# Kernel optimization log

Measured on AMD Instinct MI355X. Metric: run time of the kernel, lower is better.

The kernel has to match this reference:

```python
import jax, jax.numpy as jnp
import numpy as np

LAMBDA_M = 1.0
NUM_GRU_LAYERS = 3

B, S, H, G = 64, 512, 768, 768


def setup_inputs() -> dict:
    key = jax.random.key(0)
    ks = jax.random.split(key, 12)
    std = 0.02
    # variable-length attention mask (all rows non-empty)
    lengths = jax.random.randint(ks[0], (B,), S // 4, S + 1)
    attention_mask = (jnp.arange(S)[None, :] < lengths[:, None]).astype(jnp.float32)
    return {
        "sentence_representation": jax.random.normal(ks[1], (B, H), jnp.float32),
        "attention_mask": attention_mask,
        "aspect_embedding": jax.random.normal(ks[2], (B, H), jnp.float32),
        "sentence_embeddings": jax.random.normal(ks[3], (B, S, H), jnp.float32),
        "ws": std * jax.random.normal(ks[4], (H, H), jnp.float32),
        "wa": std * jax.random.normal(ks[5], (H, H), jnp.float32),
        "w": std * jax.random.normal(ks[6], (H,), jnp.float32),
        "whs": std * jax.random.normal(ks[7], (H, G), jnp.float32),
        "wd1": std * jax.random.normal(ks[8], (H, H), jnp.float32),
        "wd": std * jax.random.normal(ks[9], (G, H), jnp.float32),
        "w_ih": std * jax.random.normal(ks[10], (3 * G, H), jnp.float32),  # GRU input weights (r,z,n)
        "w_hh": std * jax.random.normal(ks[11], (3 * G, G), jnp.float32),  # GRU hidden weights (r,z,n)
    }


def _gru_cell(x, h, w_ih, w_hh):
    # standard GRU cell, bias=False (torch gate order: r, z, n)
    gi = x @ w_ih.T  # (B, 3G)
    gh = h @ w_hh.T  # (B, 3G)
    i_r, i_z, i_n = jnp.split(gi, 3, axis=-1)
    h_r, h_z, h_n = jnp.split(gh, 3, axis=-1)
    r = jax.nn.sigmoid(i_r + h_r)
    z = jax.nn.sigmoid(i_z + h_z)
    n = jnp.tanh(i_n + r * h_n)
    return (1.0 - z) * n + z * h


def reference(sentence_representation, attention_mask, aspect_embedding,
              sentence_embeddings, ws, wa, w, whs, wd1, wd, w_ih, w_hh):
    # Hoist loop-invariant projections (same math as recomputing per layer)
    Se = jnp.einsum('bsh,hk->bsk', sentence_embeddings, ws)  # (B,S,H)
    A = aspect_embedding @ wa                                 # (B,H)
    mask = attention_mask                                     # (B,S)
    denom = mask.sum(-1, keepdims=True)                       # (B,1)
    h = sentence_representation
    for t in range(NUM_GRU_LAYERS):
        Wd = wd1 if t == 0 else wd
        M = Se + (h @ Wd)[:, None, :] + A[:, None, :]         # (B,S,H)
        scores = jnp.tanh(M) @ w                              # (B,S)
        m = jax.nn.softmax(LAMBDA_M * scores, axis=-1)        # (B,S)
        # reweighted masked-mean pooling
        at = jnp.einsum('bs,bsh->bh', m * mask, sentence_embeddings) / denom
        if t == 0:
            h = h @ whs                                       # project to GRU hidden dim
        h = _gru_cell(at, h, w_ih, w_hh)
    return h
```

## Files before the change

kernel.cpp:

```cpp
#include <hip/hip_runtime.h>
#include <hip/hip_bf16.h>
#include <stdint.h>

#define Bdim 64
#define Sdim 512
#define Hdim 768
#define G3   2304

typedef float f32x4 __attribute__((ext_vector_type(4)));
typedef short s16x8 __attribute__((ext_vector_type(8)));
typedef short s16x4 __attribute__((ext_vector_type(4)));

__device__ __forceinline__ float bf2f(unsigned short u){
  union { unsigned int i; float f; } c; c.i = ((unsigned int)u) << 16; return c.f;
}
__device__ __forceinline__ unsigned short f2bf(float f){
  union { float f; unsigned int i; } c; c.f = f;
  unsigned int x = c.i;
  return (unsigned short)((x + 0x7fffu + ((x >> 16) & 1u)) >> 16);
}
__device__ __forceinline__ float fast_tanh(float x){
  float e = __expf(2.f * x);
  return 1.f - 2.f / (e + 1.f);
}
__device__ __forceinline__ float fast_sigmoid(float x){
  return 1.f / (1.f + __expf(-x));
}
__device__ __forceinline__ void gload16(const void* g, void* l){
  __builtin_amdgcn_global_load_lds((const __attribute__((address_space(1))) void*)g,
                                   (__attribute__((address_space(3))) void*)l, 16, 0, 0);
}

__global__ __launch_bounds__(256) void k_prep(const float* __restrict__ SE, unsigned short* __restrict__ SEb,
                                              const float* __restrict__ ws_, unsigned short* __restrict__ wsbT,
                                              const float* __restrict__ wd1, unsigned short* __restrict__ wd1T,
                                              const float* __restrict__ wd,  unsigned short* __restrict__ wdT,
                                              const float* __restrict__ wa,  unsigned short* __restrict__ waT,
                                              const float* __restrict__ whs, unsigned short* __restrict__ whsT,
                                              const float* __restrict__ w_ih, unsigned short* __restrict__ w_ihb,
                                              const float* __restrict__ w_hh, unsigned short* __restrict__ w_hhb,
                                              const float* __restrict__ sr,  unsigned short* __restrict__ srb,
                                              const float* __restrict__ asp, unsigned short* __restrict__ aspb){
  __shared__ float tile[32][33];
  int bid = blockIdx.x;
  if (bid < 2880) {
    int which = bid / 576, r = bid % 576;
    const float* src; unsigned short* dst;
    switch (which) {
      case 0: src = ws_; dst = wsbT; break;
      case 1: src = wd1; dst = wd1T; break;
      case 2: src = wd;  dst = wdT;  break;
      case 3: src = wa;  dst = waT;  break;
      default: src = whs; dst = whsT; break;
    }
    int bx = (r % 24) * 32, by = (r / 24) * 32;
    int tx = threadIdx.x % 32, ty = threadIdx.x / 32;
    for (int j = ty; j < 32; j += 8) tile[j][tx] = src[(size_t)(by + j) * Hdim + bx + tx];
    __syncthreads();
    for (int j = ty; j < 32; j += 8) dst[(size_t)(bx + j) * Hdim + by + tx] = f2bf(tile[tx][j]);
    return;
  }
  bid -= 2880;
  const float* s; unsigned short* d; int j;
  if      (bid < 12288) { s = SE;   d = SEb;   j = bid * 256 + threadIdx.x; }
  else if (bid < 13152) { s = w_ih; d = w_ihb; j = (bid - 12288) * 256 + threadIdx.x; }
  else if (bid < 14016) { s = w_hh; d = w_hhb; j = (bid - 13152) * 256 + threadIdx.x; }
  else if (bid < 14040) { s = sr;   d = srb;   j = (bid - 14016) * 256 + threadIdx.x; }
  else                  { s = asp;  d = aspb;  j = (bid - 14040) * 256 + threadIdx.x; }
  const float4* sp = (const float4*)s;
  float4 a = sp[2*j], b = sp[2*j+1];
  uint4 o;
  o.x = (unsigned)f2bf(a.x) | ((unsigned)f2bf(a.y) << 16);
  o.y = (unsigned)f2bf(a.z) | ((unsigned)f2bf(a.w) << 16);
  o.z = (unsigned)f2bf(b.x) | ((unsigned)f2bf(b.y) << 16);
  o.w = (unsigned)f2bf(b.z) | ((unsigned)f2bf(b.w) << 16);
  ((uint4*)d)[j] = o;
}

__global__ __launch_bounds__(256) void k_conv_bf16(const float* __restrict__ src,
                                                   unsigned short* __restrict__ dst, int n8){
  int i = blockIdx.x * 256 + threadIdx.x;
  if (i >= n8) return;
  const float4* s = (const float4*)src;
  float4 a = s[2*i], b = s[2*i+1];
  uint4 o;
  o.x = (unsigned)f2bf(a.x) | ((unsigned)f2bf(a.y) << 16);
  o.y = (unsigned)f2bf(a.z) | ((unsigned)f2bf(a.w) << 16);
  o.z = (unsigned)f2bf(b.x) | ((unsigned)f2bf(b.y) << 16);
  o.w = (unsigned)f2bf(b.z) | ((unsigned)f2bf(b.w) << 16);
  ((uint4*)dst)[i] = o;
}

__global__ __launch_bounds__(256) void k_conv4(const float* __restrict__ s0, unsigned short* __restrict__ d0, int c0,
                                               const float* __restrict__ s1, unsigned short* __restrict__ d1, int c1,
                                               const float* __restrict__ s2, unsigned short* __restrict__ d2, int c2,
                                               const float* __restrict__ s3, unsigned short* __restrict__ d3, int c3){
  int i = blockIdx.x * 256 + threadIdx.x;
  const float* s; unsigned short* d; int j;
  if (i < c0) { s = s0; d = d0; j = i; }
  else if (i < c0 + c1) { s = s1; d = d1; j = i - c0; }
  else if (i < c0 + c1 + c2) { s = s2; d = d2; j = i - c0 - c1; }
  else if (i < c0 + c1 + c2 + c3) { s = s3; d = d3; j = i - c0 - c1 - c2; }
  else return;
  const float4* sp = (const float4*)s;
  float4 a = sp[2*j], b = sp[2*j+1];
  uint4 o;
  o.x = (unsigned)f2bf(a.x) | ((unsigned)f2bf(a.y) << 16);
  o.y = (unsigned)f2bf(a.z) | ((unsigned)f2bf(a.w) << 16);
  o.z = (unsigned)f2bf(b.x) | ((unsigned)f2bf(b.y) << 16);
  o.w = (unsigned)f2bf(b.z) | ((unsigned)f2bf(b.w) << 16);
  ((uint4*)d)[j] = o;
}

__global__ __launch_bounds__(256) void k_transpose_ws(const float* __restrict__ src,
                                                      unsigned short* __restrict__ dst){
  __shared__ float tile[32][33];
  int bx = blockIdx.x * 32, by = blockIdx.y * 32;
  int tx = threadIdx.x % 32, ty = threadIdx.x / 32;
  for (int j = ty; j < 32; j += 8) tile[j][tx] = src[(size_t)(by + j) * Hdim + bx + tx];
  __syncthreads();
  for (int j = ty; j < 32; j += 8) dst[(size_t)(bx + j) * Hdim + by + tx] = f2bf(tile[tx][j]);
}

__global__ __launch_bounds__(256) void k_transpose4(const float* __restrict__ s0, unsigned short* __restrict__ d0,
                                                    const float* __restrict__ s1, unsigned short* __restrict__ d1,
                                                    const float* __restrict__ s2, unsigned short* __restrict__ d2,
                                                    const float* __restrict__ s3, unsigned short* __restrict__ d3){
  const float* src; unsigned short* dst;
  switch (blockIdx.z) {
    case 0: src = s0; dst = d0; break;
    case 1: src = s1; dst = d1; break;
    case 2: src = s2; dst = d2; break;
    default: src = s3; dst = d3; break;
  }
  __shared__ float tile[32][33];
  int bx = blockIdx.x * 32, by = blockIdx.y * 32;
  int tx = threadIdx.x % 32, ty = threadIdx.x / 32;
  for (int j = ty; j < 32; j += 8) tile[j][tx] = src[(size_t)(by + j) * Hdim + bx + tx];
  __syncthreads();
  for (int j = ty; j < 32; j += 8) dst[(size_t)(bx + j) * Hdim + by + tx] = f2bf(tile[tx][j]);
}

__global__ __launch_bounds__(256) void k_gemm_se(const unsigned short* __restrict__ A,
                                                 const unsigned short* __restrict__ Bt,
                                                 unsigned short* __restrict__ C){
  __shared__ unsigned short As[128 * 64];
  __shared__ unsigned short Bs[128 * 64];
  const int t = threadIdx.x;
  const int lane = t & 63;
  const int w = t >> 6, wr = w >> 1, wc = w & 1;
  int bid = blockIdx.x;
  int swz = (bid & 7) * 192 + (bid >> 3);
  const int m0 = (swz / 6) * 128, n0 = (swz % 6) * 128;

  f32x4 acc[4][4];
  #pragma unroll
  for (int m = 0; m < 4; m++)
    #pragma unroll
    for (int n = 0; n < 4; n++) acc[m][n] = (f32x4){0.f, 0.f, 0.f, 0.f};

  for (int k0 = 0; k0 < Hdim; k0 += 64) {
    #pragma unroll
    for (int i = 0; i < 4; i++) {
      int L = t * 16 + i * 4096;
      int row = L >> 7;
      int offp = L & 127;
      int goff = offp ^ ((row & 7) << 4);
      int wub = __builtin_amdgcn_readfirstlane((t & 192) * 16 + i * 4096);
      gload16((const char*)A  + ((size_t)(m0 + row) * Hdim + k0) * 2 + goff, (char*)As + wub);
      gload16((const char*)Bt + ((size_t)(n0 + row) * Hdim + k0) * 2 + goff, (char*)Bs + wub);
    }
    __syncthreads();
    #pragma unroll
    for (int kk = 0; kk < 2; kk++) {
      s16x8 af[4], bfr[4];
      #pragma unroll
      for (int m = 0; m < 4; m++) {
        int row = wr * 64 + m * 16 + (lane & 15);
        int sw = (row & 7) << 4;
        int kb = kk * 64 + (lane >> 4) * 8;
        s16x4 lo = *(const s16x4*)((const char*)As + row * 128 + (kb ^ sw));
        s16x4 hi = *(const s16x4*)((const char*)As + row * 128 + ((kb + 32) ^ sw));
        af[m] = __builtin_shufflevector(lo, hi, 0, 1, 2, 3, 4, 5, 6, 7);
      }
      #pragma unroll
      for (int n = 0; n < 4; n++) {
        int row = wc * 64 + n * 16 + (lane & 15);
        int sw = (row & 7) << 4;
        int kb = kk * 64 + (lane >> 4) * 8;
        s16x4 lo = *(const s16x4*)((const char*)Bs + row * 128 + (kb ^ sw));
        s16x4 hi = *(const s16x4*)((const char*)Bs + row * 128 + ((kb + 32) ^ sw));
        bfr[n] = __builtin_shufflevector(lo, hi, 0, 1, 2, 3, 4, 5, 6, 7);
      }
      #pragma unroll
      for (int m = 0; m < 4; m++)
        #pragma unroll
        for (int n = 0; n < 4; n++)
          acc[m][n] = __builtin_amdgcn_mfma_f32_16x16x32_bf16(af[m], bfr[n], acc[m][n], 0, 0, 0);
    }
    __syncthreads();
  }
  #pragma unroll
  for (int m = 0; m < 4; m++) {
    int rowb = m0 + wr * 64 + m * 16 + (lane >> 4) * 4;
    #pragma unroll
    for (int n = 0; n < 4; n++) {
      int col = n0 + wc * 64 + n * 16 + (lane & 15);
      #pragma unroll
      for (int r = 0; r < 4; r++)
        C[(size_t)(rowb + r) * Hdim + col] = f2bf(acc[m][n][r]);
    }
  }
}

__device__ __forceinline__ void smallM_body(const unsigned short* __restrict__ A,
                                            const unsigned short* __restrict__ Bt,
                                            float* __restrict__ C, unsigned short* __restrict__ Cb,
                                            char* ldsbuf, int n0){
  unsigned short* As = (unsigned short*)ldsbuf;
  unsigned short* Bs = (unsigned short*)(ldsbuf + 8192);
  const int t = threadIdx.x, lane = t & 63, w = t >> 6;
  f32x4 acc[4][2];
  #pragma unroll
  for (int m = 0; m < 4; m++)
    #pragma unroll
    for (int n = 0; n < 2; n++) acc[m][n] = (f32x4){0.f, 0.f, 0.f, 0.f};

  for (int k0 = 0; k0 < Hdim; k0 += 64) {
    #pragma unroll
    for (int i = 0; i < 2; i++) {
      int L = t * 16 + i * 4096, row = L >> 7, off = L & 127;
      *(uint4*)((char*)As + row * 128 + (off ^ ((row & 7) << 4))) =
        *(const uint4*)((const char*)A + ((size_t)row * Hdim + k0) * 2 + off);
    }
    #pragma unroll
    for (int i = 0; i < 4; i++) {
      int L = t * 16 + i * 4096, row = L >> 7, off = L & 127;
      *(uint4*)((char*)Bs + row * 128 + (off ^ ((row & 7) << 4))) =
        *(const uint4*)((const char*)Bt + ((size_t)(n0 + row) * Hdim + k0) * 2 + off);
    }
    __syncthreads();
    #pragma unroll
    for (int kk = 0; kk < 2; kk++) {
      s16x8 af[4], bfr[2];
      int kb = kk * 64 + (lane >> 4) * 8;
      #pragma unroll
      for (int m = 0; m < 4; m++) {
        int row = m * 16 + (lane & 15);
        int sw = (row & 7) << 4;
        s16x4 lo = *(const s16x4*)((const char*)As + row * 128 + (kb ^ sw));
        s16x4 hi = *(const s16x4*)((const char*)As + row * 128 + ((kb + 32) ^ sw));
        af[m] = __builtin_shufflevector(lo, hi, 0, 1, 2, 3, 4, 5, 6, 7);
      }
      #pragma unroll
      for (int n = 0; n < 2; n++) {
        int row = w * 32 + n * 16 + (lane & 15);
        int sw = (row & 7) << 4;
        s16x4 lo = *(const s16x4*)((const char*)Bs + row * 128 + (kb ^ sw));
        s16x4 hi = *(const s16x4*)((const char*)Bs + row * 128 + ((kb + 32) ^ sw));
        bfr[n] = __builtin_shufflevector(lo, hi, 0, 1, 2, 3, 4, 5, 6, 7);
      }
      #pragma unroll
      for (int m = 0; m < 4; m++)
        #pragma unroll
        for (int n = 0; n < 2; n++)
          acc[m][n] = __builtin_amdgcn_mfma_f32_16x16x32_bf16(af[m], bfr[n], acc[m][n], 0, 0, 0);
    }
    __syncthreads();
  }
  #pragma unroll
  for (int m = 0; m < 4; m++) {
    int rowb = m * 16 + (lane >> 4) * 4;
    #pragma unroll
    for (int n = 0; n < 2; n++) {
      int col = n0 + w * 32 + n * 16 + (lane & 15);
      #pragma unroll
      for (int r = 0; r < 4; r++) {
        float v = acc[m][n][r];
        C[(size_t)(rowb + r) * Hdim + col] = v;
        if (Cb) Cb[(size_t)(rowb + r) * Hdim + col] = f2bf(v);
      }
    }
  }
}

__device__ __forceinline__ void vpart_body(const unsigned short* __restrict__ A1,
                                           const unsigned short* __restrict__ B1t,
                                           const unsigned short* __restrict__ A2,
                                           const unsigned short* __restrict__ B2t,
                                           float* __restrict__ Vp,
                                           char* ldsbuf, int n0, int kc){
  unsigned short* As = (unsigned short*)ldsbuf;
  unsigned short* Bs = (unsigned short*)(ldsbuf + 8192);
  const int t = threadIdx.x, lane = t & 63, w = t >> 6;
  f32x4 acc[4][2];
  #pragma unroll
  for (int m = 0; m < 4; m++)
    #pragma unroll
    for (int n = 0; n < 2; n++) acc[m][n] = (f32x4){0.f, 0.f, 0.f, 0.f};

  #pragma unroll
  for (int gi = 0; gi < 4; gi++) {
    int g = kc * 4 + gi;
    const unsigned short* A  = (g < 12) ? A1 : A2;
    const unsigned short* Bt = (g < 12) ? B1t : B2t;
    int k0 = (g % 12) * 64;
    #pragma unroll
    for (int i = 0; i < 2; i++) {
      int L = t * 16 + i * 4096, row = L >> 7, off = L & 127;
      *(uint4*)((char*)As + row * 128 + (off ^ ((row & 7) << 4))) =
        *(const uint4*)((const char*)A + ((size_t)row * Hdim + k0) * 2 + off);
    }
    #pragma unroll
    for (int i = 0; i < 4; i++) {
      int L = t * 16 + i * 4096, row = L >> 7, off = L & 127;
      *(uint4*)((char*)Bs + row * 128 + (off ^ ((row & 7) << 4))) =
        *(const uint4*)((const char*)Bt + ((size_t)(n0 + row) * Hdim + k0) * 2 + off);
    }
    __syncthreads();
    #pragma unroll
    for (int kk = 0; kk < 2; kk++) {
      s16x8 af[4], bfr[2];
      int kb = kk * 64 + (lane >> 4) * 8;
      #pragma unroll
      for (int m = 0; m < 4; m++) {
        int row = m * 16 + (lane & 15);
        int sw = (row & 7) << 4;
        s16x4 lo = *(const s16x4*)((const char*)As + row * 128 + (kb ^ sw));
        s16x4 hi = *(const s16x4*)((const char*)As + row * 128 + ((kb + 32) ^ sw));
        af[m] = __builtin_shufflevector(lo, hi, 0, 1, 2, 3, 4, 5, 6, 7);
      }
      #pragma unroll
      for (int n = 0; n < 2; n++) {
        int row = w * 32 + n * 16 + (lane & 15);
        int sw = (row & 7) << 4;
        s16x4 lo = *(const s16x4*)((const char*)Bs + row * 128 + (kb ^ sw));
        s16x4 hi = *(const s16x4*)((const char*)Bs + row * 128 + ((kb + 32) ^ sw));
        bfr[n] = __builtin_shufflevector(lo, hi, 0, 1, 2, 3, 4, 5, 6, 7);
      }
      #pragma unroll
      for (int m = 0; m < 4; m++)
        #pragma unroll
        for (int n = 0; n < 2; n++)
          acc[m][n] = __builtin_amdgcn_mfma_f32_16x16x32_bf16(af[m], bfr[n], acc[m][n], 0, 0, 0);
    }
    __syncthreads();
  }
  float* outp = Vp + (size_t)kc * (Bdim * Hdim);
  #pragma unroll
  for (int m = 0; m < 4; m++) {
    int rowb = m * 16 + (lane >> 4) * 4;
    #pragma unroll
    for (int n = 0; n < 2; n++) {
      int col = n0 + w * 32 + n * 16 + (lane & 15);
      #pragma unroll
      for (int r = 0; r < 4; r++)
        outp[(size_t)(rowb + r) * Hdim + col] = acc[m][n][r];
    }
  }
}

__global__ __launch_bounds__(256) void k_vpart(const unsigned short* __restrict__ A1,
                                               const unsigned short* __restrict__ B1t,
                                               const unsigned short* __restrict__ A2,
                                               const unsigned short* __restrict__ B2t,
                                               float* __restrict__ Vp){
  __shared__ char lds[24576];
  vpart_body(A1, B1t, A2, B2t, Vp, lds, blockIdx.x * 128, blockIdx.y);
}

__global__ __launch_bounds__(256) void k_init2(const unsigned short* __restrict__ srb,
                                               const unsigned short* __restrict__ whsT,
                                               float* __restrict__ hA, unsigned short* __restrict__ hbA,
                                               const unsigned short* __restrict__ wd1T,
                                               const unsigned short* __restrict__ aspb,
                                               const unsigned short* __restrict__ waT,
                                               float* __restrict__ Vp){
  __shared__ char lds[24576];
  if (blockIdx.y == 6) smallM_body(srb, whsT, hA, hbA, lds, blockIdx.x * 128);
  else                 vpart_body(srb, wd1T, aspb, waT, Vp, lds, blockIdx.x * 128, blockIdx.y);
}

__global__ __launch_bounds__(256) void k_scores(const unsigned short* __restrict__ Seb,
                                                const float* __restrict__ Vp,
                                                const float* __restrict__ wv,
                                                float* __restrict__ scores){
  int b = blockIdx.y;
  int s_base = blockIdx.x * 16;
  int t = threadIdx.x, lane = t & 63, w = t >> 6;
  f32x4 v0 = {0,0,0,0}, v1 = {0,0,0,0}, v2 = {0,0,0,0};
  #pragma unroll
  for (int kc = 0; kc < 6; kc++) {
    const float* Vb = Vp + ((size_t)kc * Bdim + b) * Hdim;
    v0 += *(const f32x4*)(Vb + lane * 8);
    v1 += *(const f32x4*)(Vb + lane * 8 + 4);
    v2 += *(const f32x4*)(Vb + 512 + lane * 4);
  }
  f32x4 w0 = *(const f32x4*)(wv + lane * 8);
  f32x4 w1 = *(const f32x4*)(wv + lane * 8 + 4);
  f32x4 w2 = *(const f32x4*)(wv + 512 + lane * 4);
  #pragma unroll
  for (int si = 0; si < 4; si++) {
    int s = s_base + w * 4 + si;
    const unsigned short* rp = Seb + ((size_t)b * Sdim + s) * Hdim;
    ushort4 p0 = *(const ushort4*)(rp + lane * 8);
    ushort4 p1 = *(const ushort4*)(rp + lane * 8 + 4);
    ushort4 p2 = *(const ushort4*)(rp + 512 + lane * 4);
    float acc;
    acc  = fast_tanh(bf2f(p0.x) + v0[0]) * w0[0];
    acc += fast_tanh(bf2f(p0.y) + v0[1]) * w0[1];
    acc += fast_tanh(bf2f(p0.z) + v0[2]) * w0[2];
    acc += fast_tanh(bf2f(p0.w) + v0[3]) * w0[3];
    acc += fast_tanh(bf2f(p1.x) + v1[0]) * w1[0];
    acc += fast_tanh(bf2f(p1.y) + v1[1]) * w1[1];
    acc += fast_tanh(bf2f(p1.z) + v1[2]) * w1[2];
    acc += fast_tanh(bf2f(p1.w) + v1[3]) * w1[3];
    acc += fast_tanh(bf2f(p2.x) + v2[0]) * w2[0];
    acc += fast_tanh(bf2f(p2.y) + v2[1]) * w2[1];
    acc += fast_tanh(bf2f(p2.z) + v2[2]) * w2[2];
    acc += fast_tanh(bf2f(p2.w) + v2[3]) * w2[3];
    #pragma unroll
    for (int o = 32; o; o >>= 1) acc += __shfl_xor(acc, o);
    if (lane == 0) scores[(size_t)b * Sdim + s] = acc;
  }
}

__global__ __launch_bounds__(192) void k_at_sm_bf16(const unsigned short* __restrict__ SEb,
                                                    const float* __restrict__ scores,
                                                    const float* __restrict__ mask,
                                                    float* __restrict__ at_part){
  int sc = blockIdx.x, b = blockIdx.y;
  int t = threadIdx.x, lane = t & 63, w = t >> 6;
  __shared__ float sbuf[512];
  __shared__ float mbuf[512];
  __shared__ float red[3], red2[3];
  __shared__ float msh[64];
  __shared__ float half0[96 * 8];
  float lmax = -1e30f;
  #pragma unroll
  for (int j = 0; j < 3; j++) {
    int idx = t + 192 * j;
    if (idx < 512) {
      float v = scores[(size_t)b * Sdim + idx];
      float mk = mask[(size_t)b * Sdim + idx];
      sbuf[idx] = v; mbuf[idx] = mk;
      lmax = fmaxf(lmax, v);
    }
  }
  #pragma unroll
  for (int o = 32; o; o >>= 1) lmax = fmaxf(lmax, __shfl_xor(lmax, o));
  if (lane == 0) red[w] = lmax;
  __syncthreads();
  float mx = fmaxf(fmaxf(red[0], red[1]), red[2]);
  float le = 0.f, lm = 0.f;
  #pragma unroll
  for (int j = 0; j < 3; j++) {
    int idx = t + 192 * j;
    if (idx < 512) {
      float e = __expf(sbuf[idx] - mx);
      le += e; lm += mbuf[idx];
      sbuf[idx] = e * mbuf[idx];
    }
  }
  #pragma unroll
  for (int o = 32; o; o >>= 1) { le += __shfl_xor(le, o); lm += __shfl_xor(lm, o); }
  __syncthreads();
  if (lane == 0) { red[w] = le; red2[w] = lm; }
  __syncthreads();
  float inv = 1.f / ((red[0] + red[1] + red[2]) * (red2[0] + red2[1] + red2[2]));
  if (t < 64) msh[t] = sbuf[sc * 64 + t] * inv;
  __syncthreads();
  int hseg = t % 96, sh = t / 96;
  const unsigned short* base = SEb + ((size_t)b * Sdim + sc * 64 + sh * 32) * Hdim + hseg * 8;
  float acc[8] = {0, 0, 0, 0, 0, 0, 0, 0};
  for (int s = 0; s < 32; s++) {
    float m = msh[sh * 32 + s];
    ushort4 a = *(const ushort4*)(base + (size_t)s * Hdim);
    ushort4 c = *(const ushort4*)(base + (size_t)s * Hdim + 4);
    acc[0] += m * bf2f(a.x); acc[1] += m * bf2f(a.y); acc[2] += m * bf2f(a.z); acc[3] += m * bf2f(a.w);
    acc[4] += m * bf2f(c.x); acc[5] += m * bf2f(c.y); acc[6] += m * bf2f(c.z); acc[7] += m * bf2f(c.w);
  }
  if (sh == 0) {
    #pragma unroll
    for (int j = 0; j < 8; j++) half0[hseg * 8 + j] = acc[j];
  }
  __syncthreads();
  if (sh == 1) {
    float* op = at_part + ((size_t)sc * Bdim + b) * Hdim + hseg * 8;
    #pragma unroll
    for (int j = 0; j < 8; j++) op[j] = acc[j] + half0[hseg * 8 + j];
  }
}

__global__ __launch_bounds__(192) void k_at_sm_f32(const float* __restrict__ SE,
                                                   const float* __restrict__ scores,
                                                   const float* __restrict__ mask,
                                                   float* __restrict__ at_part){
  int sc = blockIdx.x, b = blockIdx.y;
  int t = threadIdx.x, lane = t & 63, w = t >> 6;
  __shared__ float sbuf[512];
  __shared__ float mbuf[512];
  __shared__ float red[3], red2[3];
  __shared__ float msh[64];
  __shared__ float half0[96 * 8];
  float lmax = -1e30f;
  #pragma unroll
  for (int j = 0; j < 3; j++) {
    int idx = t + 192 * j;
    if (idx < 512) {
      float v = scores[(size_t)b * Sdim + idx];
      float mk = mask[(size_t)b * Sdim + idx];
      sbuf[idx] = v; mbuf[idx] = mk;
      lmax = fmaxf(lmax, v);
    }
  }
  #pragma unroll
  for (int o = 32; o; o >>= 1) lmax = fmaxf(lmax, __shfl_xor(lmax, o));
  if (lane == 0) red[w] = lmax;
  __syncthreads();
  float mx = fmaxf(fmaxf(red[0], red[1]), red[2]);
  float le = 0.f, lm = 0.f;
  #pragma unroll
  for (int j = 0; j < 3; j++) {
    int idx = t + 192 * j;
    if (idx < 512) {
      float e = __expf(sbuf[idx] - mx);
      le += e; lm += mbuf[idx];
      sbuf[idx] = e * mbuf[idx];
    }
  }
  #pragma unroll
  for (int o = 32; o; o >>= 1) { le += __shfl_xor(le, o); lm += __shfl_xor(lm, o); }
  __syncthreads();
  if (lane == 0) { red[w] = le; red2[w] = lm; }
  __syncthreads();
  float inv = 1.f / ((red[0] + red[1] + red[2]) * (red2[0] + red2[1] + red2[2]));
  if (t < 64) msh[t] = sbuf[sc * 64 + t] * inv;
  __syncthreads();
  int hseg = t % 96, sh = t / 96;
  const float* base = SE + ((size_t)b * Sdim + sc * 64 + sh * 32) * Hdim + hseg * 8;
  float acc[8] = {0, 0, 0, 0, 0, 0, 0, 0};
  for (int s = 0; s < 32; s++) {
    float m = msh[sh * 32 + s];
    float4 a = *(const float4*)(base + (size_t)s * Hdim);
    float4 c = *(const float4*)(base + (size_t)s * Hdim + 4);
    acc[0] += m * a.x; acc[1] += m * a.y; acc[2] += m * a.z; acc[3] += m * a.w;
    acc[4] += m * c.x; acc[5] += m * c.y; acc[6] += m * c.z; acc[7] += m * c.w;
  }
  if (sh == 0) {
    #pragma unroll
    for (int j = 0; j < 8; j++) half0[hseg * 8 + j] = acc[j];
  }
  __syncthreads();
  if (sh == 1) {
    float* op = at_part + ((size_t)sc * Bdim + b) * Hdim + hseg * 8;
    #pragma unroll
    for (int j = 0; j < 8; j++) op[j] = acc[j] + half0[hseg * 8 + j];
  }
}

__global__ __launch_bounds__(256) void k_at_reduce(const float* __restrict__ at_part,
                                                   unsigned short* __restrict__ atb){
  int i = blockIdx.x * 256 + threadIdx.x;
  float s = 0.f;
  #pragma unroll
  for (int p = 0; p < 8; p++) s += at_part[(size_t)p * (Bdim * Hdim) + i];
  atb[i] = f2bf(s);
}

__global__ __launch_bounds__(256) void k_gates2(const unsigned short* __restrict__ atb,
                                                const unsigned short* __restrict__ hb,
                                                const unsigned short* __restrict__ w_ihb,
                                                const unsigned short* __restrict__ w_hhb,
                                                float* __restrict__ gi2,
                                                float* __restrict__ gh2){
  __shared__ unsigned short As[64 * 64];
  __shared__ unsigned short Bs[128 * 64];
  const int t = threadIdx.x, lane = t & 63, w = t >> 6;
  const int n0 = blockIdx.x * 128;
  const int z = blockIdx.y, kc = blockIdx.z;
  const unsigned short* A  = z ? hb : atb;
  const unsigned short* Bt = z ? w_hhb : w_ihb;
  float* outp = (z ? gh2 : gi2) + (size_t)kc * (Bdim * G3);
  f32x4 acc[4][2];
  #pragma unroll
  for (int m = 0; m < 4; m++)
    #pragma unroll
    for (int n = 0; n < 2; n++) acc[m][n] = (f32x4){0.f, 0.f, 0.f, 0.f};

  for (int it = 0; it < 6; it++) {
    int k0 = kc * 384 + it * 64;
    #pragma unroll
    for (int i = 0; i < 2; i++) {
      int L = t * 16 + i * 4096, row = L >> 7, off = L & 127;
      *(uint4*)((char*)As + row * 128 + (off ^ ((row & 7) << 4))) =
        *(const uint4*)((const char*)A + ((size_t)row * Hdim + k0) * 2 + off);
    }
    #pragma unroll
    for (int i = 0; i < 4; i++) {
      int L = t * 16 + i * 4096, row = L >> 7, off = L & 127;
      *(uint4*)((char*)Bs + row * 128 + (off ^ ((row & 7) << 4))) =
        *(const uint4*)((const char*)Bt + ((size_t)(n0 + row) * Hdim + k0) * 2 + off);
    }
    __syncthreads();
    #pragma unroll
    for (int kk = 0; kk < 2; kk++) {
      s16x8 af[4], bfr[2];
      int kb = kk * 64 + (lane >> 4) * 8;
      #pragma unroll
      for (int m = 0; m < 4; m++) {
        int row = m * 16 + (lane & 15);
        int sw = (row & 7) << 4;
        s16x4 lo = *(const s16x4*)((const char*)As + row * 128 + (kb ^ sw));
        s16x4 hi = *(const s16x4*)((const char*)As + row * 128 + ((kb + 32) ^ sw));
        af[m] = __builtin_shufflevector(lo, hi, 0, 1, 2, 3, 4, 5, 6, 7);
      }
      #pragma unroll
      for (int n = 0; n < 2; n++) {
        int row = w * 32 + n * 16 + (lane & 15);
        int sw = (row & 7) << 4;
        s16x4 lo = *(const s16x4*)((const char*)Bs + row * 128 + (kb ^ sw));
        s16x4 hi = *(const s16x4*)((const char*)Bs + row * 128 + ((kb + 32) ^ sw));
        bfr[n] = __builtin_shufflevector(lo, hi, 0, 1, 2, 3, 4, 5, 6, 7);
      }
      #pragma unroll
      for (int m = 0; m < 4; m++)
        #pragma unroll
        for (int n = 0; n < 2; n++)
          acc[m][n] = __builtin_amdgcn_mfma_f32_16x16x32_bf16(af[m], bfr[n], acc[m][n], 0, 0, 0);
    }
    __syncthreads();
  }
  #pragma unroll
  for (int m = 0; m < 4; m++) {
    int rowb = m * 16 + (lane >> 4) * 4;
    #pragma unroll
    for (int n = 0; n < 2; n++) {
      int col = n0 + w * 32 + n * 16 + (lane & 15);
      #pragma unroll
      for (int r = 0; r < 4; r++)
        outp[(size_t)(rowb + r) * G3 + col] = acc[m][n][r];
    }
  }
}

__global__ __launch_bounds__(256) void k_gru_elem2(const float* __restrict__ gi2,
                                                   const float* __restrict__ gh2,
                                                   const float* __restrict__ h,
                                                   float* __restrict__ hout,
                                                   unsigned short* __restrict__ hbout){
  int i = blockIdx.x * 256 + threadIdx.x;
  int b = i / Hdim, g = i % Hdim;
  const size_t P = (size_t)Bdim * G3;
  const float* gia = gi2 + (size_t)b * G3;
  const float* gha = gh2 + (size_t)b * G3;
  float ir = gia[g] + gia[P + g];
  float iz = gia[Hdim + g] + gia[P + Hdim + g];
  float in_ = gia[2 * Hdim + g] + gia[P + 2 * Hdim + g];
  float hr = gha[g] + gha[P + g];
  float hz = gha[Hdim + g] + gha[P + Hdim + g];
  float hn = gha[2 * Hdim + g] + gha[P + 2 * Hdim + g];
  float r = fast_sigmoid(ir + hr);
  float z = fast_sigmoid(iz + hz);
  float n = fast_tanh(in_ + r * hn);
  float ho = (1.f - z) * n + z * h[i];
  hout[i] = ho;
  hbout[i] = f2bf(ho);
}

extern "C" void kernel_launch(void* const* d_in, const int* in_sizes, int n_in,
                              void* d_out, int out_size, void* d_ws, size_t ws_size,
                              hipStream_t stream) {
  const float* sr   = (const float*)d_in[0];
  const float* mask = (const float*)d_in[1];
  const float* asp  = (const float*)d_in[2];
  const float* SE   = (const float*)d_in[3];
  const float* ws_  = (const float*)d_in[4];
  const float* wa   = (const float*)d_in[5];
  const float* wv   = (const float*)d_in[6];
  const float* whs  = (const float*)d_in[7];
  const float* wd1  = (const float*)d_in[8];
  const float* wd   = (const float*)d_in[9];
  const float* w_ih = (const float*)d_in[10];
  const float* w_hh = (const float*)d_in[11];
  float* out = (float*)d_out;

  char* p = (char*)d_ws;
  size_t offA = 0;
  auto A_ = [&](size_t b) -> char* { char* r = p + offA; offA += b; return r; };
  unsigned short* Seb  = (unsigned short*)A_(50331648);
  unsigned short* wsbT = (unsigned short*)A_(1179648);
  unsigned short* SEb  = (unsigned short*)A_(50331648);

  const size_t othersBytes = 18100224;
  bool keepSEb = (offA + othersBytes) <= ws_size;
  char* q = keepSEb ? (p + offA) : (char*)SEb;
  size_t o2 = 0;
  auto B_ = [&](size_t b) -> char* { char* r = q + o2; o2 += b; return r; };
  unsigned short* w_ihb = (unsigned short*)B_(3538944);
  unsigned short* w_hhb = (unsigned short*)B_(3538944);
  unsigned short* wd1T  = (unsigned short*)B_(1179648);
  unsigned short* wdT   = (unsigned short*)B_(1179648);
  unsigned short* waT   = (unsigned short*)B_(1179648);
  unsigned short* whsT  = (unsigned short*)B_(1179648);
  unsigned short* srb   = (unsigned short*)B_(98304);
  unsigned short* aspb  = (unsigned short*)B_(98304);
  float* Vp      = (float*)B_(1179648);
  float* scores  = (float*)B_(131072);
  float* at_part = (float*)B_(1572864);
  unsigned short* atb = (unsigned short*)B_(98304);
  float* gi2     = (float*)B_(1179648);
  float* gh2     = (float*)B_(1179648);
  float* hA      = (float*)B_(196608);
  float* hB      = (float*)B_(196608);
  unsigned short* hbA = (unsigned short*)B_(98304);
  unsigned short* hbB = (unsigned short*)B_(98304);
  if (!keepSEb && (offA > ws_size)) return;

  if (keepSEb) {
    k_prep<<<dim3(16944), dim3(256), 0, stream>>>(SE, SEb, ws_, wsbT, wd1, wd1T, wd, wdT,
                                                  wa, waT, whs, whsT, w_ih, w_ihb, w_hh, w_hhb,
                                                  sr, srb, asp, aspb);
    k_gemm_se<<<dim3(1536), dim3(256), 0, stream>>>(SEb, wsbT, Seb);
  } else {
    k_conv_bf16<<<dim3(12288), dim3(256), 0, stream>>>(SE, SEb, 3145728);
    k_transpose_ws<<<dim3(24, 24), dim3(256), 0, stream>>>(ws_, wsbT);
    k_gemm_se<<<dim3(1536), dim3(256), 0, stream>>>(SEb, wsbT, Seb);
    k_transpose4<<<dim3(24, 24, 4), dim3(256), 0, stream>>>(wd1, wd1T, wd, wdT, wa, waT, whs, whsT);
    k_conv4<<<dim3(1776), dim3(256), 0, stream>>>(w_ih, w_ihb, 221184, w_hh, w_hhb, 221184,
                                                  sr, srb, 6144, asp, aspb, 6144);
  }
  k_init2<<<dim3(6, 7), dim3(256), 0, stream>>>(srb, whsT, hA, hbA, wd1T, aspb, waT, Vp);

  const float* hcur = hA;
  const unsigned short* hbcur = hbA;
  for (int tl = 0; tl < 3; ++tl) {
    if (tl > 0)
      k_vpart<<<dim3(6, 6), dim3(256), 0, stream>>>(hbcur, wdT, aspb, waT, Vp);
    k_scores<<<dim3(32, 64), dim3(256), 0, stream>>>(Seb, Vp, wv, scores);
    if (keepSEb)
      k_at_sm_bf16<<<dim3(8, 64), dim3(192), 0, stream>>>(SEb, scores, mask, at_part);
    else
      k_at_sm_f32<<<dim3(8, 64), dim3(192), 0, stream>>>(SE, scores, mask, at_part);
    k_at_reduce<<<dim3(192), dim3(256), 0, stream>>>(at_part, atb);
    k_gates2<<<dim3(18, 2, 2), dim3(256), 0, stream>>>(atb, hbcur, w_ihb, w_hhb, gi2, gh2);
    float* hout = (tl == 2) ? out : ((hcur == hA) ? hB : hA);
    unsigned short* hbout = (hbcur == hbA) ? hbB : hbA;
    k_gru_elem2<<<dim3(192), dim3(256), 0, stream>>>(gi2, gh2, hcur, hout, hbout);
    hcur = hout;
    hbcur = hbout;
  }
}
```

Baseline: 238.2 us.

## Fuse at-reduction into pooling kernel and overlap hidden-gate GEMM with scores

The separate k_at_reduce launch is removed. The last of the eight pooling blocks per batch row, detected with an atomic counter and thread fence, now sums the partials and writes the bf16 attention vector. The h·W_hh gate GEMM moves out of the combined gates kernel into extra blocks of the scores kernel, since it depends only on h, leaving a smaller W_ih-only GEMM. This cuts two launches per layer and overlaps independent work, at the cost of atomics, a memset, and 64 mostly idle extra blocks in the scores grid.

```diff
diff --git a/kernel.cpp b/kernel.cpp
--- a/kernel.cpp
+++ b/kernel.cpp
@@ -360,6 +360,75 @@
   }
 }
 
+__device__ __forceinline__ void gates_body(const unsigned short* __restrict__ A,
+                                           const unsigned short* __restrict__ Bt,
+                                           float* __restrict__ outp,
+                                           char* ldsbuf, int n0, int kc){
+  unsigned short* As = (unsigned short*)ldsbuf;
+  unsigned short* Bs = (unsigned short*)(ldsbuf + 8192);
+  const int t = threadIdx.x, lane = t & 63, w = t >> 6;
+  f32x4 acc[4][2];
+  #pragma unroll
+  for (int m = 0; m < 4; m++)
+    #pragma unroll
+    for (int n = 0; n < 2; n++) acc[m][n] = (f32x4){0.f, 0.f, 0.f, 0.f};
+
+  for (int it = 0; it < 6; it++) {
+    int k0 = kc * 384 + it * 64;
+    #pragma unroll
+    for (int i = 0; i < 2; i++) {
+      int L = t * 16 + i * 4096, row = L >> 7, off = L & 127;
+      *(uint4*)((char*)As + row * 128 + (off ^ ((row & 7) << 4))) =
+        *(const uint4*)((const char*)A + ((size_t)row * Hdim + k0) * 2 + off);
+    }
+    #pragma unroll
+    for (int i = 0; i < 4; i++) {
+      int L = t * 16 + i * 4096, row = L >> 7, off = L & 127;
+      *(uint4*)((char*)Bs + row * 128 + (off ^ ((row & 7) << 4))) =
+        *(const uint4*)((const char*)Bt + ((size_t)(n0 + row) * Hdim + k0) * 2 + off);
+    }
+    __syncthreads();
+    #pragma unroll
+    for (int kk = 0; kk < 2; kk++) {
+      s16x8 af[4], bfr[2];
+      int kb = kk * 64 + (lane >> 4) * 8;
+      #pragma unroll
+      for (int m = 0; m < 4; m++) {
+        int row = m * 16 + (lane & 15);
+        int sw = (row & 7) << 4;
+        s16x4 lo = *(const s16x4*)((const char*)As + row * 128 + (kb ^ sw));
+        s16x4 hi = *(const s16x4*)((const char*)As + row * 128 + ((kb + 32) ^ sw));
+        af[m] = __builtin_shufflevector(lo, hi, 0, 1, 2, 3, 4, 5, 6, 7);
+      }
+      #pragma unroll
+      for (int n = 0; n < 2; n++) {
+        int row = w * 32 + n * 16 + (lane & 15);
+        int sw = (row & 7) << 4;
+        s16x4 lo = *(const s16x4*)((const char*)Bs + row * 128 + (kb ^ sw));
+        s16x4 hi = *(const s16x4*)((const char*)Bs + row * 128 + ((kb + 32) ^ sw));
+        bfr[n] = __builtin_shufflevector(lo, hi, 0, 1, 2, 3, 4, 5, 6, 7);
+      }
+      #pragma unroll
+      for (int m = 0; m < 4; m++)
+        #pragma unroll
+        for (int n = 0; n < 2; n++)
+          acc[m][n] = __builtin_amdgcn_mfma_f32_16x16x32_bf16(af[m], bfr[n], acc[m][n], 0, 0, 0);
+    }
+    __syncthreads();
+  }
+  #pragma unroll
+  for (int m = 0; m < 4; m++) {
+    int rowb = m * 16 + (lane >> 4) * 4;
+    #pragma unroll
+    for (int n = 0; n < 2; n++) {
+      int col = n0 + w * 32 + n * 16 + (lane & 15);
+      #pragma unroll
+      for (int r = 0; r < 4; r++)
+        outp[(size_t)(rowb + r) * G3 + col] = acc[m][n][r];
+    }
+  }
+}
+
 __global__ __launch_bounds__(256) void k_vpart(const unsigned short* __restrict__ A1,
                                                const unsigned short* __restrict__ B1t,
                                                const unsigned short* __restrict__ A2,
@@ -381,10 +450,21 @@
   else                 vpart_body(srb, wd1T, aspb, waT, Vp, lds, blockIdx.x * 128, blockIdx.y);
 }
 
-__global__ __launch_bounds__(256) void k_scores(const unsigned short* __restrict__ Seb,
-                                                const float* __restrict__ Vp,
-                                                const float* __restrict__ wv,
-                                                float* __restrict__ scores){
+__global__ __launch_bounds__(256) void k_scores_gh(const unsigned short* __restrict__ Seb,
+                                                   const float* __restrict__ Vp,
+                                                   const float* __restrict__ wv,
+                                                   float* __restrict__ scores,
+                                                   const unsigned short* __restrict__ hb,
+                                                   const unsigned short* __restrict__ w_hhb,
+                                                   float* __restrict__ gh2){
+  __shared__ char lds[24576];
+  if (blockIdx.x == 32) {
+    int idx = blockIdx.y;
+    if (idx >= 36) return;
+    int kc = idx / 18, nb = idx % 18;
+    gates_body(hb, w_hhb, gh2 + (size_t)kc * (Bdim * G3), lds, nb * 128, kc);
+    return;
+  }
   int b = blockIdx.y;
   int s_base = blockIdx.x * 16;
   int t = threadIdx.x, lane = t & 63, w = t >> 6;
@@ -428,7 +508,9 @@
 __global__ __launch_bounds__(192) void k_at_sm_bf16(const unsigned short* __restrict__ SEb,
                                                     const float* __restrict__ scores,
                                                     const float* __restrict__ mask,
-                                                    float* __restrict__ at_part){
+                                                    float* __restrict__ at_part,
+                                                    unsigned short* __restrict__ atb,
+                                                    int* __restrict__ cnt){
   int sc = blockIdx.x, b = blockIdx.y;
   int t = threadIdx.x, lane = t & 63, w = t >> 6;
   __shared__ float sbuf[512];
@@ -436,6 +518,7 @@
   __shared__ float red[3], red2[3];
   __shared__ float msh[64];
   __shared__ float half0[96 * 8];
+  __shared__ int lastflag;
   float lmax = -1e30f;
   #pragma unroll
   for (int j = 0; j < 3; j++) {
@@ -490,12 +573,27 @@
     #pragma unroll
     for (int j = 0; j < 8; j++) op[j] = acc[j] + half0[hseg * 8 + j];
   }
+  __threadfence();
+  __syncthreads();
+  if (t == 0) lastflag = atomicAdd(&cnt[b], 1);
+  __syncthreads();
+  if (lastflag == 7) {
+    __threadfence();
+    for (int col = t; col < Hdim; col += 192) {
+      float s = 0.f;
+      #pragma unroll
+      for (int p = 0; p < 8; p++) s += at_part[((size_t)p * Bdim + b) * Hdim + col];
+      atb[(size_t)b * Hdim + col] = f2bf(s);
+    }
+  }
 }
 
 __global__ __launch_bounds__(192) void k_at_sm_f32(const float* __restrict__ SE,
                                                    const float* __restrict__ scores,
                                                    const float* __restrict__ mask,
-                                                   float* __restrict__ at_part){
+                                                   float* __restrict__ at_part,
+                                                   unsigned short* __restrict__ atb,
+                                                   int* __restrict__ cnt){
   int sc = blockIdx.x, b = blockIdx.y;
   int t = threadIdx.x, lane = t & 63, w = t >> 6;
   __shared__ float sbuf[512];
@@ -503,6 +601,7 @@
   __shared__ float red[3], red2[3];
   __shared__ float msh[64];
   __shared__ float half0[96 * 8];
+  __shared__ int lastflag;
   float lmax = -1e30f;
   #pragma unroll
   for (int j = 0; j < 3; j++) {
@@ -557,91 +656,27 @@
     #pragma unroll
     for (int j = 0; j < 8; j++) op[j] = acc[j] + half0[hseg * 8 + j];
   }
-}
-
-__global__ __launch_bounds__(256) void k_at_reduce(const float* __restrict__ at_part,
-                                                   unsigned short* __restrict__ atb){
-  int i = blockIdx.x * 256 + threadIdx.x;
-  float s = 0.f;
-  #pragma unroll
-  for (int p = 0; p < 8; p++) s += at_part[(size_t)p * (Bdim * Hdim) + i];
-  atb[i] = f2bf(s);
-}
-
-__global__ __launch_bounds__(256) void k_gates2(const unsigned short* __restrict__ atb,
-                                                const unsigned short* __restrict__ hb,
-                                                const unsigned short* __restrict__ w_ihb,
-                                                const unsigned short* __restrict__ w_hhb,
-                                                float* __restrict__ gi2,
-                                                float* __restrict__ gh2){
-  __shared__ unsigned short As[64 * 64];
-  __shared__ unsigned short Bs[128 * 64];
-  const int t = threadIdx.x, lane = t & 63, w = t >> 6;
-  const int n0 = blockIdx.x * 128;
-  const int z = blockIdx.y, kc = blockIdx.z;
-  const unsigned short* A  = z ? hb : atb;
-  const unsigned short* Bt = z ? w_hhb : w_ihb;
-  float* outp = (z ? gh2 : gi2) + (size_t)kc * (Bdim * G3);
-  f32x4 acc[4][2];
-  #pragma unroll
-  for (int m = 0; m < 4; m++)
-    #pragma unroll
-    for (int n = 0; n < 2; n++) acc[m][n] = (f32x4){0.f, 0.f, 0.f, 0.f};
-
-  for (int it = 0; it < 6; it++) {
-    int k0 = kc * 384 + it * 64;
-    #pragma unroll
-    for (int i = 0; i < 2; i++) {
-      int L = t * 16 + i * 4096, row = L >> 7, off = L & 127;
-      *(uint4*)((char*)As + row * 128 + (off ^ ((row & 7) << 4))) =
-        *(const uint4*)((const char*)A + ((size_t)row * Hdim + k0) * 2 + off);
-    }
-    #pragma unroll
-    for (int i = 0; i < 4; i++) {
-      int L = t * 16 + i * 4096, row = L >> 7, off = L & 127;
-      *(uint4*)((char*)Bs + row * 128 + (off ^ ((row & 7) << 4))) =
-        *(const uint4*)((const char*)Bt + ((size_t)(n0 + row) * Hdim + k0) * 2 + off);
-    }
-    __syncthreads();
-    #pragma unroll
-    for (int kk = 0; kk < 2; kk++) {
-      s16x8 af[4], bfr[2];
-      int kb = kk * 64 + (lane >> 4) * 8;
-      #pragma unroll
-      for (int m = 0; m < 4; m++) {
-        int row = m * 16 + (lane & 15);
-        int sw = (row & 7) << 4;
-        s16x4 lo = *(const s16x4*)((const char*)As + row * 128 + (kb ^ sw));
-        s16x4 hi = *(const s16x4*)((const char*)As + row * 128 + ((kb + 32) ^ sw));
-        af[m] = __builtin_shufflevector(lo, hi, 0, 1, 2, 3, 4, 5, 6, 7);
-      }
-      #pragma unroll
-      for (int n = 0; n < 2; n++) {
-        int row = w * 32 + n * 16 + (lane & 15);
-        int sw = (row & 7) << 4;
-        s16x4 lo = *(const s16x4*)((const char*)Bs + row * 128 + (kb ^ sw));
-        s16x4 hi = *(const s16x4*)((const char*)Bs + row * 128 + ((kb + 32) ^ sw));
-        bfr[n] = __builtin_shufflevector(lo, hi, 0, 1, 2, 3, 4, 5, 6, 7);
-      }
-      #pragma unroll
-      for (int m = 0; m < 4; m++)
-        #pragma unroll
-        for (int n = 0; n < 2; n++)
-          acc[m][n] = __builtin_amdgcn_mfma_f32_16x16x32_bf16(af[m], bfr[n], acc[m][n], 0, 0, 0);
-    }
-    __syncthreads();
-  }
-  #pragma unroll
-  for (int m = 0; m < 4; m++) {
-    int rowb = m * 16 + (lane >> 4) * 4;
-    #pragma unroll
-    for (int n = 0; n < 2; n++) {
-      int col = n0 + w * 32 + n * 16 + (lane & 15);
-      #pragma unroll
-      for (int r = 0; r < 4; r++)
-        outp[(size_t)(rowb + r) * G3 + col] = acc[m][n][r];
-    }
-  }
+  __threadfence();
+  __syncthreads();
+  if (t == 0) lastflag = atomicAdd(&cnt[b], 1);
+  __syncthreads();
+  if (lastflag == 7) {
+    __threadfence();
+    for (int col = t; col < Hdim; col += 192) {
+      float s = 0.f;
+      #pragma unroll
+      for (int p = 0; p < 8; p++) s += at_part[((size_t)p * Bdim + b) * Hdim + col];
+      atb[(size_t)b * Hdim + col] = f2bf(s);
+    }
+  }
+}
+
+__global__ __launch_bounds__(256) void k_gates_gi(const unsigned short* __restrict__ atb,
+                                                  const unsigned short* __restrict__ w_ihb,
+                                                  float* __restrict__ gi2){
+  __shared__ char lds[24576];
+  int kc = blockIdx.y;
+  gates_body(atb, w_ihb, gi2 + (size_t)kc * (Bdim * G3), lds, blockIdx.x * 128, kc);
 }
 
 __global__ __launch_bounds__(256) void k_gru_elem2(const float* __restrict__ gi2,
@@ -690,6 +725,7 @@
   auto A_ = [&](size_t b) -> char* { char* r = p + offA; offA += b; return r; };
   unsigned short* Seb  = (unsigned short*)A_(50331648);
   unsigned short* wsbT = (unsigned short*)A_(1179648);
+  int* cnt = (int*)A_(1024);
   unsigned short* SEb  = (unsigned short*)A_(50331648);
 
   const size_t othersBytes = 18100224;
@@ -717,6 +753,8 @@
   unsigned short* hbB = (unsigned short*)B_(98304);
   if (!keepSEb && (offA > ws_size)) return;
 
+  hipMemsetAsync(cnt, 0, 3 * 64 * sizeof(int), stream);
+
   if (keepSEb) {
     k_prep<<<dim3(16944), dim3(256), 0, stream>>>(SE, SEb, ws_, wsbT, wd1, wd1T, wd, wdT,
                                                   wa, waT, whs, whsT, w_ih, w_ihb, w_hh, w_hhb,
@@ -737,13 +775,12 @@
   for (int tl = 0; tl < 3; ++tl) {
     if (tl > 0)
       k_vpart<<<dim3(6, 6), dim3(256), 0, stream>>>(hbcur, wdT, aspb, waT, Vp);
-    k_scores<<<dim3(32, 64), dim3(256), 0, stream>>>(Seb, Vp, wv, scores);
+    k_scores_gh<<<dim3(33, 64), dim3(256), 0, stream>>>(Seb, Vp, wv, scores, hbcur, w_hhb, gh2);
     if (keepSEb)
-      k_at_sm_bf16<<<dim3(8, 64), dim3(192), 0, stream>>>(SEb, scores, mask, at_part);
+      k_at_sm_bf16<<<dim3(8, 64), dim3(192), 0, stream>>>(SEb, scores, mask, at_part, atb, cnt + tl * 64);
     else
-      k_at_sm_f32<<<dim3(8, 64), dim3(192), 0, stream>>>(SE, scores, mask, at_part);
-    k_at_reduce<<<dim3(192), dim3(256), 0, stream>>>(at_part, atb);
-    k_gates2<<<dim3(18, 2, 2), dim3(256), 0, stream>>>(atb, hbcur, w_ihb, w_hhb, gi2, gh2);
+      k_at_sm_f32<<<dim3(8, 64), dim3(192), 0, stream>>>(SE, scores, mask, at_part, atb, cnt + tl * 64);
+    k_gates_gi<<<dim3(18, 2), dim3(256), 0, stream>>>(atb, w_ihb, gi2);
     float* hout = (tl == 2) ? out : ((hcur == hA) ? hB : hA);
     unsigned short* hbout = (hbcur == hbA) ? hbB : hbA;
     k_gru_elem2<<<dim3(192), dim3(256), 0, stream>>>(gi2, gh2, hcur, hout, hbout);
```

Measured after the change: 401.2 us. 68.4% more time.
